# Kernel optimization log

Measured on AMD Instinct MI355X. Metric: run time of the kernel, lower is better.

Reference implementation:

```python
import jax, jax.numpy as jnp
import numpy as np

B, N, C, H = 4, 1024, 1024, 16
HD = C // H  # 64
THETA = 10000.0


def _rope_cos_sin(n, hd, theta):
    # classic 1D RoPE cache; [n, hd] with each freq repeated twice (interleaved pairs)
    inv_freq = 1.0 / theta ** (jnp.arange(0, hd, 2, dtype=jnp.float32) / hd)
    t = jnp.arange(n, dtype=jnp.float32)
    freqs = t[:, None] * inv_freq[None, :]              # [n, hd/2]
    cos = jnp.repeat(jnp.cos(freqs), 2, axis=-1)        # [n, hd]
    sin = jnp.repeat(jnp.sin(freqs), 2, axis=-1)
    # original clones & forces row 0 to identity rotation (already true since t=0)
    cos = cos.at[0].set(1.0)
    sin = sin.at[0].set(0.0)
    return cos, sin


def _rotate_half(x):
    # interleaved rotate-half: (x0,x1,x2,x3,...) -> (-x1,x0,-x3,x2,...)
    x1 = x[..., 0::2]
    x2 = x[..., 1::2]
    return jnp.stack((-x2, x1), axis=-1).reshape(x.shape)


def setup_inputs() -> dict:
    key = jax.random.key(0)
    ks = jax.random.split(key, 5)
    s = 0.02
    return {
        "x": jax.random.normal(ks[0], (B, N, C), dtype=jnp.float32),
        "qkv_w": jax.random.normal(ks[1], (3 * C, C), dtype=jnp.float32) * s,
        "qkv_b": jax.random.normal(ks[2], (3 * C,), dtype=jnp.float32) * s,
        "proj_w": jax.random.normal(ks[3], (C, C), dtype=jnp.float32) * s,
        "proj_b": jax.random.normal(ks[4], (C,), dtype=jnp.float32) * s,
    }


def reference(x, qkv_w, qkv_b, proj_w, proj_b):
    b, n, c = x.shape
    h, hd = H, HD
    qkv = x @ qkv_w.T + qkv_b                              # [b, n, 3c]
    qkv = qkv.reshape(b, n, 3, h, hd).transpose(2, 0, 3, 1, 4)  # [3, b, h, n, hd]
    q, k, v = qkv[0], qkv[1], qkv[2]
    scale = hd ** -0.5
    q = q * scale                                          # explicit pre-scale (as in source)
    cos, sin = _rope_cos_sin(n, hd, THETA)                 # [n, hd]
    cos = cos[None, None]                                  # broadcast over b, h
    sin = sin[None, None]
    q = q * cos + _rotate_half(q) * sin
    k = k * cos + _rotate_half(k) * sin
    # F.scaled_dot_product_attention also applies its default 1/sqrt(hd) scale
    logits = jnp.einsum('bhqd,bhkd->bhqk', q, k) * scale   # [b, h, n, n]
    attn = jax.nn.softmax(logits, axis=-1)
    out = jnp.einsum('bhqk,bhkd->bhqd', attn, v)           # [b, h, n, hd]
    out = out.transpose(0, 2, 1, 3).reshape(b, n, c)
    return out @ proj_w.T + proj_b
```

## Files before the change

### kernel.cpp

```cpp
#include <hip/hip_runtime.h>
#include <hip/hip_bf16.h>
#include <stdint.h>

#define DEVI __device__ __forceinline__

typedef __attribute__((ext_vector_type(8))) short short8;
typedef __attribute__((ext_vector_type(4))) short short4v;
typedef __attribute__((ext_vector_type(4))) float floatx4;

DEVI ushort f2bf(float f) {
  union { float f; uint32_t u; } v; v.f = f;
  uint32_t u = v.u;
  uint32_t r = (u + 0x7FFFu + ((u >> 16) & 1u)) >> 16;
  return (ushort)r;
}
DEVI ushort f2bf_fast(float f) {
  union { float f; uint32_t u; } v; v.f = f;
  return (ushort)((v.u + 0x8000u) >> 16);
}
DEVI float bf2f(ushort h) {
  union { uint32_t u; float f; } v; v.u = ((uint32_t)h) << 16;
  return v.f;
}
DEVI void gld_lds16(const void* g, void* l) {
  __builtin_amdgcn_global_load_lds(
      (const __attribute__((address_space(1))) unsigned int*)g,
      (__attribute__((address_space(3))) unsigned int*)l, 16, 0, 0);
}

__global__ __launch_bounds__(256, 4) void cast_all(
    const float* __restrict__ x, const float* __restrict__ w1,
    const float* __restrict__ w2, ushort* __restrict__ xb,
    ushort* __restrict__ w1b, ushort* __restrict__ w2b) {
  const int N1 = 4096 * 1024, N2 = 3072 * 1024, N3 = 1024 * 1024;
  int i = (blockIdx.x * 256 + threadIdx.x) * 4;
  const int total = N1 + N2 + N3;
  int stride = gridDim.x * 256 * 4;
  for (; i < total; i += stride) {
    const float* src; ushort* dst; int off;
    if (i < N1) { src = x; dst = xb; off = i; }
    else if (i < N1 + N2) { src = w1; dst = w1b; off = i - N1; }
    else { src = w2; dst = w2b; off = i - N1 - N2; }
    float4 v = *(const float4*)(src + off);
    ushort4 o;
    o.x = f2bf(v.x); o.y = f2bf(v.y); o.z = f2bf(v.z); o.w = f2bf(v.w);
    *(ushort4*)(dst + off) = o;
  }
}

__global__ __launch_bounds__(256, 4) void rope_table(float2* __restrict__ tab) {
  int id = blockIdx.x * 256 + threadIdx.x;
  int j = id & 31, n = id >> 5;
  float inv = powf(10000.0f, -(float)(2 * j) / 64.0f);
  float fr = (float)n * inv;
  tab[id] = make_float2(cosf(fr), sinf(fr));
}

__global__ __launch_bounds__(256, 2) void gemm_qkv(
    const ushort* __restrict__ A, const ushort* __restrict__ Bm,
    const float* __restrict__ bias, const float2* __restrict__ tab,
    ushort* __restrict__ Qb, ushort* __restrict__ Kb,
    ushort* __restrict__ Vsrc) {
  const int K = 1024;
  __shared__ ushort As[2][128 * 32];
  __shared__ ushort Bs[2][128 * 32];
  const int tid = threadIdx.x;
  const int w = tid >> 6, lane = tid & 63;

  const int bid = blockIdx.x;
  const int xcd = bid & 7, i5 = bid >> 3;
  const int lm = i5 & 7, ln = i5 >> 3;
  const int mt = (xcd & 3) * 8 + lm;
  const int nt = (xcd >> 2) * 12 + ln;
  const int m0 = mt * 128, n0 = nt * 128;

  const int wm = (w >> 1) * 64, wn = (w & 1) * 64;
  const int lrow = lane & 15, lk = (lane >> 4) * 8;

  const ushort* agp = A + (size_t)(m0 + w * 32 + (lane >> 2)) * K + (lane & 3) * 8;
  const ushort* bgp = Bm + (size_t)(n0 + w * 32 + (lane >> 2)) * K + (lane & 3) * 8;
  const int stoff = (w * 32) * 32 + lane * 8;

  auto STAGE = [&](const int buf) {
    gld_lds16(agp, &As[buf][0] + stoff);
    gld_lds16(agp + 16 * K, &As[buf][0] + stoff + 16 * 32);
    gld_lds16(bgp, &Bs[buf][0] + stoff);
    gld_lds16(bgp + 16 * K, &Bs[buf][0] + stoff + 16 * 32);
    agp += 32; bgp += 32;
  };

  floatx4 acc[4][4] = {};

  auto TILE = [&](const int buf) {
    short8 af[4], bf[4];
#pragma unroll
    for (int t = 0; t < 4; ++t) {
      af[t] = *(const short8*)(&As[buf][0] + (wm + t * 16 + lrow) * 32 + lk);
      bf[t] = *(const short8*)(&Bs[buf][0] + (wn + t * 16 + lrow) * 32 + lk);
    }
#pragma unroll
    for (int i = 0; i < 4; ++i)
#pragma unroll
      for (int j = 0; j < 4; ++j)
        acc[i][j] = __builtin_amdgcn_mfma_f32_16x16x32_bf16(af[i], bf[j], acc[i][j], 0, 0, 0);
  };

  STAGE(0);
  asm volatile("s_waitcnt vmcnt(0)" ::: "memory");
  __builtin_amdgcn_s_barrier();
  __builtin_amdgcn_sched_barrier(0);

  for (int k0 = 0; k0 < 32; k0 += 2) {
    if (k0 + 1 < 32) STAGE(1);
    __builtin_amdgcn_sched_barrier(0);
    TILE(0);
    asm volatile("s_waitcnt vmcnt(0)" ::: "memory");
    __builtin_amdgcn_s_barrier();
    __builtin_amdgcn_sched_barrier(0);

    if (k0 + 2 < 32) STAGE(0);
    __builtin_amdgcn_sched_barrier(0);
    TILE(1);
    asm volatile("s_waitcnt vmcnt(0)" ::: "memory");
    __builtin_amdgcn_s_barrier();
    __builtin_amdgcn_sched_barrier(0);
  }

  const int role = n0 >> 10;
  const float sc = (1.0f / 64.0f) * 1.44269504088896f;
#pragma unroll
  for (int i = 0; i < 4; ++i) {
    int mrow = m0 + wm + i * 16 + (lane >> 4) * 4;
#pragma unroll
    for (int j = 0; j < 4; ++j) {
      int ncol = n0 + wn + j * 16 + (lane & 15);
      float bv = bias[ncol];
      int cm = ncol & 1023;
      int h = cm >> 6, d = cm & 63;
#pragma unroll
      for (int r = 0; r < 4; ++r) {
        float v = acc[i][j][r] + bv;
        int row = mrow + r;
        int b = row >> 10, n = row & 1023;
        if (role == 2) {
          Vsrc[(size_t)row * 1024 + cm] = f2bf(v);
        } else {
          float p = __shfl_xor(v, 1);
          float2 cs = tab[n * 32 + (d >> 1)];
          float o = (d & 1) ? (v * cs.x + p * cs.y) : (v * cs.x - p * cs.y);
          if (role == 0) o *= sc;
          ushort* dst = (role == 0) ? Qb : Kb;
          dst[((size_t)(b * 16 + h) * 1024 + n) * 64 + d] = f2bf(o);
        }
      }
    }
  }
}

__global__ __launch_bounds__(256, 2) void gemm_proj(
    const ushort* __restrict__ A, const ushort* __restrict__ Bm,
    const float* __restrict__ bias, float* __restrict__ Cout) {
  const int K = 1024;
  __shared__ ushort As[2][128 * 32];
  __shared__ ushort Bs[2][128 * 32];
  const int tid = threadIdx.x;
  const int w = tid >> 6, lane = tid & 63;

  const int bid = blockIdx.x;
  const int xcd = bid & 7, i5 = bid >> 3;
  const int lm = i5 & 7, ln = i5 >> 3;
  const int mt = (xcd & 3) * 8 + lm;
  const int nt = (xcd >> 2) * 4 + ln;
  const int m0 = mt * 128, n0 = nt * 128;

  const int wm = (w >> 1) * 64, wn = (w & 1) * 64;
  const int lrow = lane & 15, lk = (lane >> 4) * 8;

  const ushort* agp = A + (size_t)(m0 + w * 32 + (lane >> 2)) * K + (lane & 3) * 8;
  const ushort* bgp = Bm + (size_t)(n0 + w * 32 + (lane >> 2)) * K + (lane & 3) * 8;
  const int stoff = (w * 32) * 32 + lane * 8;

  auto STAGE = [&](const int buf) {
    gld_lds16(agp, &As[buf][0] + stoff);
    gld_lds16(agp + 16 * K, &As[buf][0] + stoff + 16 * 32);
    gld_lds16(bgp, &Bs[buf][0] + stoff);
    gld_lds16(bgp + 16 * K, &Bs[buf][0] + stoff + 16 * 32);
    agp += 32; bgp += 32;
  };

  floatx4 acc[4][4] = {};

  auto TILE = [&](const int buf) {
    short8 af[4], bf[4];
#pragma unroll
    for (int t = 0; t < 4; ++t) {
      af[t] = *(const short8*)(&As[buf][0] + (wm + t * 16 + lrow) * 32 + lk);
      bf[t] = *(const short8*)(&Bs[buf][0] + (wn + t * 16 + lrow) * 32 + lk);
    }
#pragma unroll
    for (int i = 0; i < 4; ++i)
#pragma unroll
      for (int j = 0; j < 4; ++j)
        acc[i][j] = __builtin_amdgcn_mfma_f32_16x16x32_bf16(af[i], bf[j], acc[i][j], 0, 0, 0);
  };

  STAGE(0);
  asm volatile("s_waitcnt vmcnt(0)" ::: "memory");
  __builtin_amdgcn_s_barrier();
  __builtin_amdgcn_sched_barrier(0);

  for (int k0 = 0; k0 < 32; k0 += 2) {
    if (k0 + 1 < 32) STAGE(1);
    __builtin_amdgcn_sched_barrier(0);
    TILE(0);
    asm volatile("s_waitcnt vmcnt(0)" ::: "memory");
    __builtin_amdgcn_s_barrier();
    __builtin_amdgcn_sched_barrier(0);

    if (k0 + 2 < 32) STAGE(0);
    __builtin_amdgcn_sched_barrier(0);
    TILE(1);
    asm volatile("s_waitcnt vmcnt(0)" ::: "memory");
    __builtin_amdgcn_s_barrier();
    __builtin_amdgcn_sched_barrier(0);
  }

#pragma unroll
  for (int i = 0; i < 4; ++i) {
    int mrow = m0 + wm + i * 16 + (lane >> 4) * 4;
#pragma unroll
    for (int j = 0; j < 4; ++j) {
      int ncol = n0 + wn + j * 16 + (lane & 15);
      float bv = bias[ncol];
#pragma unroll
      for (int r = 0; r < 4; ++r)
        Cout[(size_t)(mrow + r) * 1024 + ncol] = acc[i][j][r] + bv;
    }
  }
}

__global__ __launch_bounds__(256, 4) void v_trans(
    const ushort* __restrict__ Vsrc, ushort* __restrict__ Vt) {
  __shared__ ushort t[64][72];
  int bh = blockIdx.y, ntile = blockIdx.x;
  int b = bh >> 4, h = bh & 15;
  int n0 = ntile * 64;
  int tid = threadIdx.x;
  int r = tid >> 2, cc = (tid & 3) * 16;
  const ushort* src = Vsrc + (size_t)(b * 1024 + n0 + r) * 1024 + h * 64 + cc;
  *(short8*)(&t[r][cc]) = *(const short8*)(src);
  *(short8*)(&t[r][cc + 8]) = *(const short8*)(src + 8);
  __syncthreads();
  int d = tid >> 2;
  ushort outv[16];
#pragma unroll
  for (int i = 0; i < 16; ++i) outv[i] = t[cc + i][d];
  ushort* dst = Vt + (size_t)bh * 65536 + (size_t)d * 1024 + n0 + cc;
  *(short8*)(dst) = *(const short8*)(outv);
  *(short8*)(dst + 8) = *(const short8*)(outv + 8);
}

__global__ __launch_bounds__(256, 4) void attn(
    const ushort* __restrict__ Q, const ushort* __restrict__ Kc,
    const ushort* __restrict__ Vt, ushort* __restrict__ AO) {
  __shared__ char lds[2][16384];
  char* ldsbase = &lds[0][0];
  int id = blockIdx.x;
  int bh = id & 63, qi = id >> 6;
  int b = bh >> 4, h = bh & 15;
  int q0 = qi * 64;
  int tid = threadIdx.x, w = tid >> 6, lane = tid & 63;
  int l15 = lane & 15, g = lane >> 4;
  const ushort* Qbh = Q + (size_t)bh * 65536;
  const char* Kbh = (const char*)(Kc + (size_t)bh * 65536);
  const char* Vbh = (const char*)(Vt + (size_t)bh * 65536);

  short8 qf[2];
#pragma unroll
  for (int ks = 0; ks < 2; ++ks)
    qf[ks] = *(const short8*)(Qbh + (size_t)(q0 + w * 16 + l15) * 64 + ks * 32 + g * 8);

  int kaddr[8];
#pragma unroll
  for (int ks = 0; ks < 2; ++ks)
#pragma unroll
    for (int nt = 0; nt < 4; ++nt) {
      int row = nt * 16 + l15;
      kaddr[ks * 4 + nt] = (row * 128 + ks * 64 + g * 16) ^ ((row & 7) << 4);
    }
  int vaddr[16];
#pragma unroll
  for (int ch = 0; ch < 2; ++ch)
#pragma unroll
    for (int dt = 0; dt < 4; ++dt)
#pragma unroll
      for (int hf = 0; hf < 2; ++hf) {
        int row = dt * 16 + l15;
        vaddr[(ch * 4 + dt) * 2 + hf] =
            8192 + ((row * 128 + ch * 64 + hf * 32 + g * 8) ^ ((row & 7) << 4));
      }

  const int d0 = w * 2048 + lane * 16;
  const int d1 = d0 + 1024;
  const int r0 = d0 >> 7, r1 = d1 >> 7;
  const int s0 = d0 ^ ((r0 & 7) << 4), s1 = d1 ^ ((r1 & 7) << 4);
  const char* pK0 = Kbh + s0;
  const char* pK1 = Kbh + s1;
  const char* pV0 = Vbh + r0 * 2048 + (s0 & 127);
  const char* pV1 = Vbh + r1 * 2048 + (s1 & 127);

  auto STAGE = [&](const int B) {
    gld_lds16(pK0, ldsbase + B + d0);
    gld_lds16(pK1, ldsbase + B + d1);
    gld_lds16(pV0, ldsbase + B + 8192 + d0);
    gld_lds16(pV1, ldsbase + B + 8192 + d1);
    pK0 += 8192; pK1 += 8192; pV0 += 128; pV1 += 128;
  };

  floatx4 oacc[4] = {};
  float lrun = 0.f;

  auto TILE = [&](const int B) {
    floatx4 sacc[4] = {};
    __builtin_amdgcn_s_setprio(1);
#pragma unroll
    for (int ks = 0; ks < 2; ++ks) {
      short8 kf[4];
#pragma unroll
      for (int nt = 0; nt < 4; ++nt)
        kf[nt] = *(const short8*)(ldsbase + B + kaddr[ks * 4 + nt]);
#pragma unroll
      for (int nt = 0; nt < 4; ++nt)
        sacc[nt] = __builtin_amdgcn_mfma_f32_16x16x32_bf16(kf[nt], qf[ks], sacc[nt], 0, 0, 0);
    }
    __builtin_amdgcn_s_setprio(0);

    float rs = 0.f;
#pragma unroll
    for (int nt = 0; nt < 4; ++nt)
#pragma unroll
      for (int r = 0; r < 4; ++r) {
        float p = __builtin_amdgcn_exp2f(sacc[nt][r]);
        sacc[nt][r] = p;
        rs += p;
      }
    lrun += rs;

    short8 pa[2];
#pragma unroll
    for (int ch = 0; ch < 2; ++ch)
#pragma unroll
      for (int r = 0; r < 4; ++r) {
        pa[ch][r] = (short)f2bf_fast(sacc[2 * ch][r]);
        pa[ch][r + 4] = (short)f2bf_fast(sacc[2 * ch + 1][r]);
      }

    __builtin_amdgcn_s_setprio(1);
#pragma unroll
    for (int ch = 0; ch < 2; ++ch)
#pragma unroll
      for (int dt = 0; dt < 4; ++dt) {
        short4v va = *(const short4v*)(ldsbase + B + vaddr[(ch * 4 + dt) * 2]);
        short4v vb = *(const short4v*)(ldsbase + B + vaddr[(ch * 4 + dt) * 2 + 1]);
        short8 vf = __builtin_shufflevector(va, vb, 0, 1, 2, 3, 4, 5, 6, 7);
        oacc[dt] = __builtin_amdgcn_mfma_f32_16x16x32_bf16(pa[ch], vf, oacc[dt], 0, 0, 0);
      }
    __builtin_amdgcn_s_setprio(0);
  };

  STAGE(0);
  asm volatile("s_waitcnt vmcnt(0)" ::: "memory");
  __builtin_amdgcn_s_barrier();
  __builtin_amdgcn_sched_barrier(0);

  for (int kt = 0; kt < 16; kt += 2) {
    STAGE(16384);
    __builtin_amdgcn_sched_barrier(0);
    TILE(0);
    asm volatile("s_waitcnt vmcnt(0)" ::: "memory");
    __builtin_amdgcn_s_barrier();
    __builtin_amdgcn_sched_barrier(0);

    if (kt + 2 < 16) STAGE(0);
    __builtin_amdgcn_sched_barrier(0);
    TILE(16384);
    asm volatile("s_waitcnt vmcnt(0)" ::: "memory");
    __builtin_amdgcn_s_barrier();
    __builtin_amdgcn_sched_barrier(0);
  }

  lrun += __shfl_xor(lrun, 16);
  lrun += __shfl_xor(lrun, 32);
  float linv = 1.0f / lrun;
  float linvR[4];
#pragma unroll
  for (int r = 0; r < 4; ++r) linvR[r] = __shfl(linv, g * 4 + r);
#pragma unroll
  for (int r = 0; r < 4; ++r) {
    int nseq = q0 + w * 16 + g * 4 + r;
#pragma unroll
    for (int dt = 0; dt < 4; ++dt) {
      int d = dt * 16 + l15;
      AO[(size_t)(b * 1024 + nseq) * 1024 + h * 64 + d] = f2bf(oacc[dt][r] * linvR[r]);
    }
  }
}

extern "C" void kernel_launch(void* const* d_in, const int* in_sizes, int n_in,
                              void* d_out, int out_size, void* d_ws, size_t ws_size,
                              hipStream_t stream) {
  const float* x = (const float*)d_in[0];
  const float* qkv_w = (const float*)d_in[1];
  const float* qkv_b = (const float*)d_in[2];
  const float* proj_w = (const float*)d_in[3];
  const float* proj_b = (const float*)d_in[4];
  float* out = (float*)d_out;

  char* ws = (char*)d_ws;
  size_t off = 0;
  auto alloc = [&](size_t bytes) -> void* {
    void* p = ws + off;
    off += (bytes + 255) & ~(size_t)255;
    return p;
  };
  ushort* xb = (ushort*)alloc(4096ull * 1024 * 2);
  ushort* wqkvb = (ushort*)alloc(3072ull * 1024 * 2);
  ushort* wprojb = (ushort*)alloc(1024ull * 1024 * 2);
  ushort* Qb = (ushort*)alloc(64ull * 1024 * 64 * 2);
  ushort* Kb = (ushort*)alloc(64ull * 1024 * 64 * 2);
  ushort* Vsrc = (ushort*)alloc(4096ull * 1024 * 2);
  ushort* Vt = (ushort*)alloc(64ull * 1024 * 64 * 2);
  ushort* AO = (ushort*)alloc(4096ull * 1024 * 2);
  float2* tab = (float2*)alloc(1024ull * 32 * sizeof(float2));

  cast_all<<<2048, 256, 0, stream>>>(x, qkv_w, proj_w, xb, wqkvb, wprojb);
  rope_table<<<128, 256, 0, stream>>>(tab);

  gemm_qkv<<<768, 256, 0, stream>>>(xb, wqkvb, qkv_b, tab, Qb, Kb, Vsrc);

  dim3 gv(16, 64);
  v_trans<<<gv, 256, 0, stream>>>(Vsrc, Vt);

  attn<<<1024, 256, 0, stream>>>(Qb, Kb, Vt, AO);

  gemm_proj<<<256, 256, 0, stream>>>(AO, wprojb, proj_b, out);
}
```

Before: 106.9 us.

## Triple-buffer LDS in QKV and projection GEMMs with one barrier per k-step

Both GEMM kernels go from double-buffered to triple-buffered LDS staging. Two stages are prefetched ahead, and each iteration waits with vmcnt(4) instead of vmcnt(0), so one tile's global loads stay in flight while the current tile computes. There is now one barrier per k-step instead of one per half-iteration. LDS use rises to 48KB per block, and the launch bound occupancy hint goes from 2 to 3 blocks, which may cap registers for the 64 accumulator floats.

After: 103.6 us. 1.03x faster.

```diff
diff --git a/kernel.cpp b/kernel.cpp
--- a/kernel.cpp
+++ b/kernel.cpp
@@ -56,14 +56,14 @@
   tab[id] = make_float2(cosf(fr), sinf(fr));
 }
 
-__global__ __launch_bounds__(256, 2) void gemm_qkv(
+__global__ __launch_bounds__(256, 3) void gemm_qkv(
     const ushort* __restrict__ A, const ushort* __restrict__ Bm,
     const float* __restrict__ bias, const float2* __restrict__ tab,
     ushort* __restrict__ Qb, ushort* __restrict__ Kb,
     ushort* __restrict__ Vsrc) {
   const int K = 1024;
-  __shared__ ushort As[2][128 * 32];
-  __shared__ ushort Bs[2][128 * 32];
+  __shared__ char lds[3][16384];
+  char* L0 = &lds[0][0];
   const int tid = threadIdx.x;
   const int w = tid >> 6, lane = tid & 63;
 
@@ -75,28 +75,30 @@
   const int m0 = mt * 128, n0 = nt * 128;
 
   const int wm = (w >> 1) * 64, wn = (w & 1) * 64;
-  const int lrow = lane & 15, lk = (lane >> 4) * 8;
+  const int lrow = lane & 15, lk2 = (lane >> 4) * 16;
 
   const ushort* agp = A + (size_t)(m0 + w * 32 + (lane >> 2)) * K + (lane & 3) * 8;
   const ushort* bgp = Bm + (size_t)(n0 + w * 32 + (lane >> 2)) * K + (lane & 3) * 8;
-  const int stoff = (w * 32) * 32 + lane * 8;
-
-  auto STAGE = [&](const int buf) {
-    gld_lds16(agp, &As[buf][0] + stoff);
-    gld_lds16(agp + 16 * K, &As[buf][0] + stoff + 16 * 32);
-    gld_lds16(bgp, &Bs[buf][0] + stoff);
-    gld_lds16(bgp + 16 * K, &Bs[buf][0] + stoff + 16 * 32);
+  const int stoff = w * 2048 + lane * 16;
+
+  auto STAGE = [&](const int base) {
+    char* L = L0 + base;
+    gld_lds16(agp, L + stoff);
+    gld_lds16(agp + 16 * K, L + stoff + 1024);
+    gld_lds16(bgp, L + 8192 + stoff);
+    gld_lds16(bgp + 16 * K, L + 8192 + stoff + 1024);
     agp += 32; bgp += 32;
   };
 
   floatx4 acc[4][4] = {};
 
-  auto TILE = [&](const int buf) {
+  auto TILE = [&](const int base) {
+    const char* L = L0 + base;
     short8 af[4], bf[4];
 #pragma unroll
     for (int t = 0; t < 4; ++t) {
-      af[t] = *(const short8*)(&As[buf][0] + (wm + t * 16 + lrow) * 32 + lk);
-      bf[t] = *(const short8*)(&Bs[buf][0] + (wn + t * 16 + lrow) * 32 + lk);
+      af[t] = *(const short8*)(L + (wm + t * 16 + lrow) * 64 + lk2);
+      bf[t] = *(const short8*)(L + 8192 + (wn + t * 16 + lrow) * 64 + lk2);
     }
 #pragma unroll
     for (int i = 0; i < 4; ++i)
@@ -106,25 +108,24 @@
   };
 
   STAGE(0);
+  STAGE(16384);
+  int bT = 0, bS = 32768;
+
+  for (int t = 0; t < 31; ++t) {
+    asm volatile("s_waitcnt vmcnt(4)" ::: "memory");
+    __builtin_amdgcn_s_barrier();
+    __builtin_amdgcn_sched_barrier(0);
+    if (t < 30) STAGE(bS);
+    __builtin_amdgcn_sched_barrier(0);
+    TILE(bT);
+    __builtin_amdgcn_sched_barrier(0);
+    bT += 16384; if (bT == 49152) bT = 0;
+    bS += 16384; if (bS == 49152) bS = 0;
+  }
   asm volatile("s_waitcnt vmcnt(0)" ::: "memory");
   __builtin_amdgcn_s_barrier();
   __builtin_amdgcn_sched_barrier(0);
-
-  for (int k0 = 0; k0 < 32; k0 += 2) {
-    if (k0 + 1 < 32) STAGE(1);
-    __builtin_amdgcn_sched_barrier(0);
-    TILE(0);
-    asm volatile("s_waitcnt vmcnt(0)" ::: "memory");
-    __builtin_amdgcn_s_barrier();
-    __builtin_amdgcn_sched_barrier(0);
-
-    if (k0 + 2 < 32) STAGE(0);
-    __builtin_amdgcn_sched_barrier(0);
-    TILE(1);
-    asm volatile("s_waitcnt vmcnt(0)" ::: "memory");
-    __builtin_amdgcn_s_barrier();
-    __builtin_amdgcn_sched_barrier(0);
-  }
+  TILE(bT);
 
   const int role = n0 >> 10;
   const float sc = (1.0f / 64.0f) * 1.44269504088896f;
@@ -157,12 +158,12 @@
   }
 }
 
-__global__ __launch_bounds__(256, 2) void gemm_proj(
+__global__ __launch_bounds__(256, 3) void gemm_proj(
     const ushort* __restrict__ A, const ushort* __restrict__ Bm,
     const float* __restrict__ bias, float* __restrict__ Cout) {
   const int K = 1024;
-  __shared__ ushort As[2][128 * 32];
-  __shared__ ushort Bs[2][128 * 32];
+  __shared__ char lds[3][16384];
+  char* L0 = &lds[0][0];
   const int tid = threadIdx.x;
   const int w = tid >> 6, lane = tid & 63;
 
@@ -174,28 +175,30 @@
   const int m0 = mt * 128, n0 = nt * 128;
 
   const int wm = (w >> 1) * 64, wn = (w & 1) * 64;
-  const int lrow = lane & 15, lk = (lane >> 4) * 8;
+  const int lrow = lane & 15, lk2 = (lane >> 4) * 16;
 
   const ushort* agp = A + (size_t)(m0 + w * 32 + (lane >> 2)) * K + (lane & 3) * 8;
   const ushort* bgp = Bm + (size_t)(n0 + w * 32 + (lane >> 2)) * K + (lane & 3) * 8;
-  const int stoff = (w * 32) * 32 + lane * 8;
-
-  auto STAGE = [&](const int buf) {
-    gld_lds16(agp, &As[buf][0] + stoff);
-    gld_lds16(agp + 16 * K, &As[buf][0] + stoff + 16 * 32);
-    gld_lds16(bgp, &Bs[buf][0] + stoff);
-    gld_lds16(bgp + 16 * K, &Bs[buf][0] + stoff + 16 * 32);
+  const int stoff = w * 2048 + lane * 16;
+
+  auto STAGE = [&](const int base) {
+    char* L = L0 + base;
+    gld_lds16(agp, L + stoff);
+    gld_lds16(agp + 16 * K, L + stoff + 1024);
+    gld_lds16(bgp, L + 8192 + stoff);
+    gld_lds16(bgp + 16 * K, L + 8192 + stoff + 1024);
     agp += 32; bgp += 32;
   };
 
   floatx4 acc[4][4] = {};
 
-  auto TILE = [&](const int buf) {
+  auto TILE = [&](const int base) {
+    const char* L = L0 + base;
     short8 af[4], bf[4];
 #pragma unroll
     for (int t = 0; t < 4; ++t) {
-      af[t] = *(const short8*)(&As[buf][0] + (wm + t * 16 + lrow) * 32 + lk);
-      bf[t] = *(const short8*)(&Bs[buf][0] + (wn + t * 16 + lrow) * 32 + lk);
+      af[t] = *(const short8*)(L + (wm + t * 16 + lrow) * 64 + lk2);
+      bf[t] = *(const short8*)(L + 8192 + (wn + t * 16 + lrow) * 64 + lk2);
     }
 #pragma unroll
     for (int i = 0; i < 4; ++i)
@@ -205,25 +208,24 @@
   };
 
   STAGE(0);
+  STAGE(16384);
+  int bT = 0, bS = 32768;
+
+  for (int t = 0; t < 31; ++t) {
+    asm volatile("s_waitcnt vmcnt(4)" ::: "memory");
+    __builtin_amdgcn_s_barrier();
+    __builtin_amdgcn_sched_barrier(0);
+    if (t < 30) STAGE(bS);
+    __builtin_amdgcn_sched_barrier(0);
+    TILE(bT);
+    __builtin_amdgcn_sched_barrier(0);
+    bT += 16384; if (bT == 49152) bT = 0;
+    bS += 16384; if (bS == 49152) bS = 0;
+  }
   asm volatile("s_waitcnt vmcnt(0)" ::: "memory");
   __builtin_amdgcn_s_barrier();
   __builtin_amdgcn_sched_barrier(0);
-
-  for (int k0 = 0; k0 < 32; k0 += 2) {
-    if (k0 + 1 < 32) STAGE(1);
-    __builtin_amdgcn_sched_barrier(0);
-    TILE(0);
-    asm volatile("s_waitcnt vmcnt(0)" ::: "memory");
-    __builtin_amdgcn_s_barrier();
-    __builtin_amdgcn_sched_barrier(0);
-
-    if (k0 + 2 < 32) STAGE(0);
-    __builtin_amdgcn_sched_barrier(0);
-    TILE(1);
-    asm volatile("s_waitcnt vmcnt(0)" ::: "memory");
-    __builtin_amdgcn_s_barrier();
-    __builtin_amdgcn_sched_barrier(0);
-  }
+  TILE(bT);
 
 #pragma unroll
   for (int i = 0; i < 4; ++i) {
```

## Deepen GEMM K-tile to 64 with XOR-swizzled LDS layout

Applied to the files above, without the earlier changes.

Both the QKV and projection GEMMs now stage 64-wide K slices (128 bytes per row) instead of 32, which halves the number of barrier and wait iterations. The shared-memory layout uses an XOR swizzle on 16-byte chunks, applied on the global side of the direct-to-LDS loads, to avoid bank conflicts on fragment reads. Each tile now runs two MFMA k-steps. LDS use doubles to 64KB per block, which may limit how many blocks fit per CU.

Result: slower. 123.4 us (+15.4%).

```diff
diff --git a/kernel.cpp b/kernel.cpp
--- a/kernel.cpp
+++ b/kernel.cpp
@@ -61,9 +61,8 @@
     const float* __restrict__ bias, const float2* __restrict__ tab,
     ushort* __restrict__ Qb, ushort* __restrict__ Kb,
     ushort* __restrict__ Vsrc) {
-  const int K = 1024;
-  __shared__ ushort As[2][128 * 32];
-  __shared__ ushort Bs[2][128 * 32];
+  __shared__ __align__(16) char As[2][16384];
+  __shared__ __align__(16) char Bs[2][16384];
   const int tid = threadIdx.x;
   const int w = tid >> 6, lane = tid & 63;
 
@@ -75,34 +74,45 @@
   const int m0 = mt * 128, n0 = nt * 128;
 
   const int wm = (w >> 1) * 64, wn = (w & 1) * 64;
-  const int lrow = lane & 15, lk = (lane >> 4) * 8;
-
-  const ushort* agp = A + (size_t)(m0 + w * 32 + (lane >> 2)) * K + (lane & 3) * 8;
-  const ushort* bgp = Bm + (size_t)(n0 + w * 32 + (lane >> 2)) * K + (lane & 3) * 8;
-  const int stoff = (w * 32) * 32 + lane * 8;
+  const int lrow = lane & 15, g = lane >> 4;
+
+  const int sw = (((lane & 7) ^ ((lane >> 3) & 7)) << 4);
+  const char* aG = (const char*)A + (size_t)(m0 + w * 32 + (lane >> 3)) * 2048 + sw;
+  const char* bG = (const char*)Bm + (size_t)(n0 + w * 32 + (lane >> 3)) * 2048 + sw;
+  const int ldst = w * 4096 + lane * 16;
 
   auto STAGE = [&](const int buf) {
-    gld_lds16(agp, &As[buf][0] + stoff);
-    gld_lds16(agp + 16 * K, &As[buf][0] + stoff + 16 * 32);
-    gld_lds16(bgp, &Bs[buf][0] + stoff);
-    gld_lds16(bgp + 16 * K, &Bs[buf][0] + stoff + 16 * 32);
-    agp += 32; bgp += 32;
+    char* LA = &As[buf][0] + ldst;
+    char* LB = &Bs[buf][0] + ldst;
+#pragma unroll
+    for (int t = 0; t < 4; ++t) {
+      gld_lds16(aG + (size_t)t * 8 * 2048, LA + t * 1024);
+      gld_lds16(bG + (size_t)t * 8 * 2048, LB + t * 1024);
+    }
+    aG += 128; bG += 128;
   };
 
   floatx4 acc[4][4] = {};
 
   auto TILE = [&](const int buf) {
-    short8 af[4], bf[4];
-#pragma unroll
-    for (int t = 0; t < 4; ++t) {
-      af[t] = *(const short8*)(&As[buf][0] + (wm + t * 16 + lrow) * 32 + lk);
-      bf[t] = *(const short8*)(&Bs[buf][0] + (wn + t * 16 + lrow) * 32 + lk);
-    }
-#pragma unroll
-    for (int i = 0; i < 4; ++i)
-#pragma unroll
-      for (int j = 0; j < 4; ++j)
-        acc[i][j] = __builtin_amdgcn_mfma_f32_16x16x32_bf16(af[i], bf[j], acc[i][j], 0, 0, 0);
+#pragma unroll
+    for (int ks = 0; ks < 2; ++ks) {
+      short8 af[4], bf[4];
+#pragma unroll
+      for (int t = 0; t < 4; ++t) {
+        int rowa = wm + t * 16 + lrow;
+        af[t] = *(const short8*)(&As[buf][0] + rowa * 128 +
+                                 ((ks * 64 + g * 16) ^ ((rowa & 7) << 4)));
+        int rowb = wn + t * 16 + lrow;
+        bf[t] = *(const short8*)(&Bs[buf][0] + rowb * 128 +
+                                 ((ks * 64 + g * 16) ^ ((rowb & 7) << 4)));
+      }
+#pragma unroll
+      for (int i = 0; i < 4; ++i)
+#pragma unroll
+        for (int j = 0; j < 4; ++j)
+          acc[i][j] = __builtin_amdgcn_mfma_f32_16x16x32_bf16(af[i], bf[j], acc[i][j], 0, 0, 0);
+    }
   };
 
   STAGE(0);
@@ -110,15 +120,15 @@
   __builtin_amdgcn_s_barrier();
   __builtin_amdgcn_sched_barrier(0);
 
-  for (int k0 = 0; k0 < 32; k0 += 2) {
-    if (k0 + 1 < 32) STAGE(1);
+  for (int t = 0; t < 16; t += 2) {
+    STAGE(1);
     __builtin_amdgcn_sched_barrier(0);
     TILE(0);
     asm volatile("s_waitcnt vmcnt(0)" ::: "memory");
     __builtin_amdgcn_s_barrier();
     __builtin_amdgcn_sched_barrier(0);
 
-    if (k0 + 2 < 32) STAGE(0);
+    if (t + 2 < 16) STAGE(0);
     __builtin_amdgcn_sched_barrier(0);
     TILE(1);
     asm volatile("s_waitcnt vmcnt(0)" ::: "memory");
@@ -160,9 +170,8 @@
 __global__ __launch_bounds__(256, 2) void gemm_proj(
     const ushort* __restrict__ A, const ushort* __restrict__ Bm,
     const float* __restrict__ bias, float* __restrict__ Cout) {
-  const int K = 1024;
-  __shared__ ushort As[2][128 * 32];
-  __shared__ ushort Bs[2][128 * 32];
+  __shared__ __align__(16) char As[2][16384];
+  __shared__ __align__(16) char Bs[2][16384];
   const int tid = threadIdx.x;
   const int w = tid >> 6, lane = tid & 63;
 
@@ -174,34 +183,45 @@
   const int m0 = mt * 128, n0 = nt * 128;
 
   const int wm = (w >> 1) * 64, wn = (w & 1) * 64;
-  const int lrow = lane & 15, lk = (lane >> 4) * 8;
-
-  const ushort* agp = A + (size_t)(m0 + w * 32 + (lane >> 2)) * K + (lane & 3) * 8;
-  const ushort* bgp = Bm + (size_t)(n0 + w * 32 + (lane >> 2)) * K + (lane & 3) * 8;
-  const int stoff = (w * 32) * 32 + lane * 8;
+  const int lrow = lane & 15, g = lane >> 4;
+
+  const int sw = (((lane & 7) ^ ((lane >> 3) & 7)) << 4);
+  const char* aG = (const char*)A + (size_t)(m0 + w * 32 + (lane >> 3)) * 2048 + sw;
+  const char* bG = (const char*)Bm + (size_t)(n0 + w * 32 + (lane >> 3)) * 2048 + sw;
+  const int ldst = w * 4096 + lane * 16;
 
   auto STAGE = [&](const int buf) {
-    gld_lds16(agp, &As[buf][0] + stoff);
-    gld_lds16(agp + 16 * K, &As[buf][0] + stoff + 16 * 32);
-    gld_lds16(bgp, &Bs[buf][0] + stoff);
-    gld_lds16(bgp + 16 * K, &Bs[buf][0] + stoff + 16 * 32);
-    agp += 32; bgp += 32;
+    char* LA = &As[buf][0] + ldst;
+    char* LB = &Bs[buf][0] + ldst;
+#pragma unroll
+    for (int t = 0; t < 4; ++t) {
+      gld_lds16(aG + (size_t)t * 8 * 2048, LA + t * 1024);
+      gld_lds16(bG + (size_t)t * 8 * 2048, LB + t * 1024);
+    }
+    aG += 128; bG += 128;
   };
 
   floatx4 acc[4][4] = {};
 
   auto TILE = [&](const int buf) {
-    short8 af[4], bf[4];
-#pragma unroll
-    for (int t = 0; t < 4; ++t) {
-      af[t] = *(const short8*)(&As[buf][0] + (wm + t * 16 + lrow) * 32 + lk);
-      bf[t] = *(const short8*)(&Bs[buf][0] + (wn + t * 16 + lrow) * 32 + lk);
-    }
-#pragma unroll
-    for (int i = 0; i < 4; ++i)
-#pragma unroll
-      for (int j = 0; j < 4; ++j)
-        acc[i][j] = __builtin_amdgcn_mfma_f32_16x16x32_bf16(af[i], bf[j], acc[i][j], 0, 0, 0);
+#pragma unroll
+    for (int ks = 0; ks < 2; ++ks) {
+      short8 af[4], bf[4];
+#pragma unroll
+      for (int t = 0; t < 4; ++t) {
+        int rowa = wm + t * 16 + lrow;
+        af[t] = *(const short8*)(&As[buf][0] + rowa * 128 +
+                                 ((ks * 64 + g * 16) ^ ((rowa & 7) << 4)));
+        int rowb = wn + t * 16 + lrow;
+        bf[t] = *(const short8*)(&Bs[buf][0] + rowb * 128 +
+                                 ((ks * 64 + g * 16) ^ ((rowb & 7) << 4)));
+      }
+#pragma unroll
+      for (int i = 0; i < 4; ++i)
+#pragma unroll
+        for (int j = 0; j < 4; ++j)
+          acc[i][j] = __builtin_amdgcn_mfma_f32_16x16x32_bf16(af[i], bf[j], acc[i][j], 0, 0, 0);
+    }
   };
 
   STAGE(0);
@@ -209,15 +229,15 @@
   __builtin_amdgcn_s_barrier();
   __builtin_amdgcn_sched_barrier(0);
 
-  for (int k0 = 0; k0 < 32; k0 += 2) {
-    if (k0 + 1 < 32) STAGE(1);
+  for (int t = 0; t < 16; t += 2) {
+    STAGE(1);
     __builtin_amdgcn_sched_barrier(0);
     TILE(0);
     asm volatile("s_waitcnt vmcnt(0)" ::: "memory");
     __builtin_amdgcn_s_barrier();
     __builtin_amdgcn_sched_barrier(0);
 
-    if (k0 + 2 < 32) STAGE(0);
+    if (t + 2 < 16) STAGE(0);
     __builtin_amdgcn_sched_barrier(0);
     TILE(1);
     asm volatile("s_waitcnt vmcnt(0)" ::: "memory");
```
